# Kernel optimization log

Hardware: AMD Instinct MI355X
Metric: run time of the kernel (lower is better)

## Reference

```python
import jax, jax.numpy as jnp
import numpy as np

B, N, D, H = 4, 1024, 768, 12
DH = D // H
HIDDEN = 4 * D
EPS = 1e-6


def _layernorm(x, g, b):
    mu = jnp.mean(x, axis=-1, keepdims=True)
    var = jnp.mean(jnp.square(x - mu), axis=-1, keepdims=True)
    return (x - mu) * jax.lax.rsqrt(var + EPS) * g + b


def setup_inputs() -> dict:
    key = jax.random.key(0)
    ks = jax.random.split(key, 8)
    s = 0.02  # init scale for weights
    return {
        "x": jax.random.normal(ks[0], (B, N, D), jnp.float32),
        "adj_bias": jax.random.normal(ks[1], (N, N), jnp.float32) * 0.1,
        "ln1_g": jnp.ones((D,), jnp.float32),
        "ln1_b": jnp.zeros((D,), jnp.float32),
        "qkv_w": jax.random.normal(ks[2], (D, 3 * D), jnp.float32) * s,
        "qkv_b": jnp.zeros((3 * D,), jnp.float32),
        "proj_w": jax.random.normal(ks[3], (D, D), jnp.float32) * s,
        "proj_b": jnp.zeros((D,), jnp.float32),
        "ln2_g": jnp.ones((D,), jnp.float32),
        "ln2_b": jnp.zeros((D,), jnp.float32),
        "fc1_w": jax.random.normal(ks[4], (D, HIDDEN), jnp.float32) * s,
        "fc1_b": jnp.zeros((HIDDEN,), jnp.float32),
        "fc2_w": jax.random.normal(ks[5], (HIDDEN, D), jnp.float32) * s,
        "fc2_b": jnp.zeros((D,), jnp.float32),
    }


def reference(x, adj_bias, ln1_g, ln1_b, qkv_w, qkv_b, proj_w, proj_b,
              ln2_g, ln2_b, fc1_w, fc1_b, fc2_w, fc2_b):
    scale = DH ** -0.5
    # --- attention with additive adjacency bias ---
    h = _layernorm(x, ln1_g, ln1_b)
    qkv = (h @ qkv_w + qkv_b).reshape(B, N, 3, H, DH)
    q, k, v = (jnp.moveaxis(qkv, 2, 0)[i].transpose(0, 2, 1, 3) for i in range(3))  # [B,H,N,DH]
    scores = jnp.einsum('bhqd,bhkd->bhqk', q, k) * scale + adj_bias[None, None]
    w = jax.nn.softmax(scores, axis=-1)
    attn = jnp.einsum('bhqk,bhkd->bhqd', w, v)          # [B,H,N,DH]
    attn = attn.transpose(0, 2, 1, 3).reshape(B, N, D)  # [B,N,D]
    x = x + (attn @ proj_w + proj_b)
    # --- MLP ---
    h2 = _layernorm(x, ln2_g, ln2_b)
    m = jax.nn.gelu(h2 @ fc1_w + fc1_b, approximate=False) @ fc2_w + fc2_b
    return x + m
```

## Files before the change

kernel.cpp:

```cpp
#include <hip/hip_runtime.h>
#include <cstdint>
#include <cstring>

typedef unsigned short u16;
typedef __attribute__((ext_vector_type(8))) short short8;
typedef __attribute__((ext_vector_type(4))) float float4v;

#define BB 4
#define NN 1024
#define DD 768
#define HH 12
#define DHH 64
#define HID 3072
#define MM (BB*NN)

__device__ __forceinline__ u16 f2b(float f) {
  unsigned int u = __float_as_uint(f);
  u += 0x7FFF + ((u >> 16) & 1);
  return (u16)(u >> 16);
}
__device__ __forceinline__ float b2f(u16 h) {
  return __uint_as_float(((unsigned int)h) << 16);
}

__device__ __forceinline__ void gll16(const void* g, void* l) {
  __builtin_amdgcn_global_load_lds(
      (const __attribute__((address_space(1))) unsigned int*)g,
      (__attribute__((address_space(3))) unsigned int*)l, 16, 0, 0);
}

__global__ __launch_bounds__(256)
void prep_k(const float* __restrict__ qkvw, const float* __restrict__ projw,
            const float* __restrict__ fc1w, const float* __restrict__ fc2w,
            const float* __restrict__ adj,
            u16* __restrict__ wtqkv, u16* __restrict__ wtproj,
            u16* __restrict__ wtfc1, u16* __restrict__ wtfc2,
            u16* __restrict__ adjP) {
  __shared__ float tile[32][33];
  const int id = blockIdx.x, t = threadIdx.x;
  if (id < 6912) {
    const float* w; u16* wt; int K, N, tid;
    if (id < 1728)      { w = qkvw;  wt = wtqkv;  K = DD;  N = 3 * DD; tid = id; }
    else if (id < 2304) { w = projw; wt = wtproj; K = DD;  N = DD;     tid = id - 1728; }
    else if (id < 4608) { w = fc1w;  wt = wtfc1;  K = DD;  N = HID;    tid = id - 2304; }
    else                { w = fc2w;  wt = wtfc2;  K = HID; N = DD;     tid = id - 4608; }
    const int ntiles = N / 32;
    const int n0 = (tid % ntiles) * 32, k0 = (tid / ntiles) * 32;
    const int tx = t & 31, ty = t >> 5;
#pragma unroll
    for (int i = 0; i < 4; i++)
      tile[ty + i * 8][tx] = w[(size_t)(k0 + ty + i * 8) * N + n0 + tx];
    __syncthreads();
#pragma unroll
    for (int i = 0; i < 4; i++)
      wt[(size_t)(n0 + ty + i * 8) * K + k0 + tx] = f2b(tile[tx][ty + i * 8]);
  } else {
    const int aid = id - 6912;
    const int qt = aid >> 4, kt = aid & 15;
    const int wv = t >> 6, q4 = (t >> 4) & 3, m15 = t & 15;
    u16 v[16];
#pragma unroll
    for (int ct = 0; ct < 4; ct++)
#pragma unroll
      for (int r = 0; r < 4; r++)
        v[ct * 4 + r] =
            f2b(adj[(size_t)(qt * 64 + wv * 16 + q4 * 4 + r) * NN + kt * 64 + ct * 16 + m15]);
    u16* dst = adjP + (size_t)aid * 4096 + t * 16;
    *(uint4*)dst = *(const uint4*)&v[0];
    *(uint4*)(dst + 8) = *(const uint4*)&v[8];
  }
}

__global__ __launch_bounds__(256)
void ln_k(const float* __restrict__ x, const float* __restrict__ g,
          const float* __restrict__ b, u16* __restrict__ o) {
  const int row = blockIdx.x, t = threadIdx.x;
  const float* xr = x + (size_t)row * DD;
  float v0 = xr[t], v1 = xr[t + 256], v2 = xr[t + 512];
  float s = v0 + v1 + v2;
  float s2 = v0 * v0 + v1 * v1 + v2 * v2;
#pragma unroll
  for (int off = 32; off > 0; off >>= 1) {
    s += __shfl_down(s, off);
    s2 += __shfl_down(s2, off);
  }
  __shared__ float rs[4], rs2[4], bc[2];
  const int lane = t & 63, wv = t >> 6;
  if (lane == 0) { rs[wv] = s; rs2[wv] = s2; }
  __syncthreads();
  if (t == 0) {
    float ts = rs[0] + rs[1] + rs[2] + rs[3];
    float ts2 = rs2[0] + rs2[1] + rs2[2] + rs2[3];
    float mean = ts * (1.f / DD);
    float var = ts2 * (1.f / DD) - mean * mean;
    bc[0] = mean;
    bc[1] = rsqrtf(var + 1e-6f);
  }
  __syncthreads();
  const float mean = bc[0], rstd = bc[1];
  u16* orow = o + (size_t)row * DD;
  orow[t]       = f2b((v0 - mean) * rstd * g[t]       + b[t]);
  orow[t + 256] = f2b((v1 - mean) * rstd * g[t + 256] + b[t + 256]);
  orow[t + 512] = f2b((v2 - mean) * rstd * g[t + 512] + b[t + 512]);
}

template <int MODE, int TN>
__global__ __launch_bounds__(256, 4)
void gemm_k(const u16* __restrict__ A, const u16* __restrict__ Bt,
            const float* __restrict__ bias, const float* __restrict__ resid,
            float* __restrict__ outf, u16* __restrict__ outb,
            u16* __restrict__ outq, u16* __restrict__ outk, u16* __restrict__ outv,
            int M, int N, int K) {
  __shared__ u16 As[2][128 * 32];
  __shared__ u16 Bs[2][TN * 32];
  constexpr int JM = TN / 32;
  constexpr int VC = (TN == 128) ? 4 : 3;
  const int gx = gridDim.x;
  const int id = blockIdx.y * gx + blockIdx.x;
  const int xcd = id & 7, rem = id >> 3;
  const int bx = rem % gx, by = (rem / gx) * 8 + xcd;
  const int tileM = by * 128, tileN = bx * TN;
  const int lane = threadIdx.x & 63, wave = threadIdx.x >> 6;
  const int wrow = (wave >> 1) * 64, wcol = (wave & 1) * (TN / 2);
  const int m15 = lane & 15, q4 = lane >> 4;

  float4v acc[4][JM];
#pragma unroll
  for (int i = 0; i < 4; i++)
#pragma unroll
    for (int j = 0; j < JM; j++) acc[i][j] = (float4v)0.f;

  auto stage = [&](int kt, int buf) {
    const int kk0 = kt * 32;
#pragma unroll
    for (int q = wave; q < 8; q += 4) {
      const int c = q * 64 + lane;
      gll16(A + (size_t)(tileM + (c >> 2)) * K + kk0 + (c & 3) * 8, &As[buf][q * 512]);
    }
#pragma unroll
    for (int q = wave; q < TN / 16; q += 4) {
      const int c = q * 64 + lane;
      gll16(Bt + (size_t)(tileN + (c >> 2)) * K + kk0 + (c & 3) * 8, &Bs[buf][q * 512]);
    }
  };

  const int T = K >> 5;
  stage(0, 0);
  for (int kt = 0; kt < T; ++kt) {
    const int cur = kt & 1;
    if (kt + 1 < T) {
      stage(kt + 1, cur ^ 1);
      asm volatile("s_waitcnt vmcnt(%0)\n\ts_barrier" :: "n"(VC) : "memory");
    } else {
      asm volatile("s_waitcnt vmcnt(0)\n\ts_barrier" ::: "memory");
    }
    short8 af[4], bfr[JM];
#pragma unroll
    for (int i = 0; i < 4; i++)
      af[i] = *(const short8*)(&As[cur][(wrow + i * 16 + m15) * 32 + q4 * 8]);
#pragma unroll
    for (int j = 0; j < JM; j++)
      bfr[j] = *(const short8*)(&Bs[cur][(wcol + j * 16 + m15) * 32 + q4 * 8]);
#pragma unroll
    for (int i = 0; i < 4; i++)
#pragma unroll
      for (int j = 0; j < JM; j++)
        acc[i][j] = __builtin_amdgcn_mfma_f32_16x16x32_bf16(af[i], bfr[j], acc[i][j], 0, 0, 0);
    asm volatile("s_waitcnt lgkmcnt(0)\n\ts_barrier" ::: "memory");
  }

#pragma unroll
  for (int i = 0; i < 4; i++) {
#pragma unroll
    for (int j = 0; j < JM; j++) {
      const int col = tileN + wcol + j * 16 + m15;
#pragma unroll
      for (int r = 0; r < 4; r++) {
        const int row = tileM + wrow + i * 16 + q4 * 4 + r;
        float v = acc[i][j][r] + bias[col];
        if (MODE == 1) {
          outf[(size_t)row * N + col] = resid[(size_t)row * N + col] + v;
        } else if (MODE == 2) {
          float gv = 0.5f * v * (1.f + erff(v * 0.70710678f));
          outb[(size_t)row * N + col] = f2b(gv);
        } else {
          const int three = col / DD, hh = (col % DD) >> 6, dh = col & 63;
          const int bb = row >> 10, nn = row & 1023;
          if (three == 2) {
            outv[(((size_t)(bb * HH + hh)) * DHH + dh) * NN + nn] = f2b(v);
          } else {
            const size_t idx = (((size_t)(bb * HH + hh)) * NN + nn) * DHH + dh;
            (three == 0 ? outq : outk)[idx] = f2b(v);
          }
        }
      }
    }
  }
}

__global__ __launch_bounds__(256, 4)
void attn_k(const u16* __restrict__ qw, const u16* __restrict__ kw,
            const u16* __restrict__ vtw, const u16* __restrict__ adjP,
            u16* __restrict__ out) {
  __shared__ u16 Ks[64][72];
  __shared__ u16 Vt[64][72];
  __shared__ u16 Pb[4][16][72];

  const int id = blockIdx.y * 16 + blockIdx.x;
  const int xcd = id & 7, rem = id >> 3;
  const int qt = rem % 16, bh = (rem / 16) * 8 + xcd;
  const int t = threadIdx.x, lane = t & 63, wave = t >> 6;
  const int m15 = lane & 15, q4 = lane >> 4;

  const u16* qrow = qw + ((size_t)bh * NN + qt * 64 + wave * 16 + m15) * DHH;
  const short8 qf0 = *(const short8*)(qrow + q4 * 8);
  const short8 qf1 = *(const short8*)(qrow + 32 + q4 * 8);

  float lreg[4] = {0.f, 0.f, 0.f, 0.f};
  float4v o[4];
#pragma unroll
  for (int ct = 0; ct < 4; ct++) o[ct] = (float4v)0.f;

  const u16* kbase0 = kw + (size_t)bh * NN * DHH;
  const u16* vtbase0 = vtw + (size_t)bh * DHH * NN;
  const u16* abase = adjP + (size_t)qt * 16 * 4096 + t * 16;

  const int r0 = t >> 3;
  const int c80 = (t & 7) * 8;

  uint4 kr0 = *(const uint4*)(kbase0 + r0 * 64 + c80);
  uint4 kr1 = *(const uint4*)(kbase0 + (r0 + 32) * 64 + c80);
  uint4 vr0 = *(const uint4*)(vtbase0 + (size_t)r0 * NN + c80);
  uint4 vr1 = *(const uint4*)(vtbase0 + (size_t)(r0 + 32) * NN + c80);

  for (int kt = 0; kt < 16; kt++) {
    __syncthreads();
    *(uint4*)&Ks[r0][c80] = kr0;
    *(uint4*)&Ks[r0 + 32][c80] = kr1;
    *(uint4*)&Vt[r0][c80] = vr0;
    *(uint4*)&Vt[r0 + 32][c80] = vr1;
    __syncthreads();
    if (kt < 15) {
      const u16* kb = kbase0 + (size_t)(kt + 1) * 64 * DHH;
      const u16* vb = vtbase0 + (kt + 1) * 64;
      kr0 = *(const uint4*)(kb + r0 * 64 + c80);
      kr1 = *(const uint4*)(kb + (r0 + 32) * 64 + c80);
      vr0 = *(const uint4*)(vb + (size_t)r0 * NN + c80);
      vr1 = *(const uint4*)(vb + (size_t)(r0 + 32) * NN + c80);
    }
    u16 av[16];
    const u16* ap = abase + (size_t)kt * 4096;
    *(uint4*)&av[0] = *(const uint4*)ap;
    *(uint4*)&av[8] = *(const uint4*)(ap + 8);

    float4v s[4];
#pragma unroll
    for (int ct = 0; ct < 4; ct++) s[ct] = (float4v)0.f;
#pragma unroll
    for (int ct = 0; ct < 4; ct++) {
      short8 b = *(const short8*)&Ks[ct * 16 + m15][q4 * 8];
      s[ct] = __builtin_amdgcn_mfma_f32_16x16x32_bf16(qf0, b, s[ct], 0, 0, 0);
    }
#pragma unroll
    for (int ct = 0; ct < 4; ct++) {
      short8 b = *(const short8*)&Ks[ct * 16 + m15][32 + q4 * 8];
      s[ct] = __builtin_amdgcn_mfma_f32_16x16x32_bf16(qf1, b, s[ct], 0, 0, 0);
    }

#pragma unroll
    for (int ct = 0; ct < 4; ct++)
#pragma unroll
      for (int r = 0; r < 4; r++) {
        float v = s[ct][r] * 0.125f + b2f(av[ct * 4 + r]);
        u16 pb = f2b(__expf(v));
        Pb[wave][q4 * 4 + r][ct * 16 + m15] = pb;
        lreg[r] += b2f(pb);
      }

    asm volatile("s_waitcnt lgkmcnt(0)" ::: "memory");

    short8 a0 = *(const short8*)&Pb[wave][m15][q4 * 8];
    short8 a1 = *(const short8*)&Pb[wave][m15][32 + q4 * 8];
#pragma unroll
    for (int ct = 0; ct < 4; ct++) {
      short8 b = *(const short8*)&Vt[ct * 16 + m15][q4 * 8];
      o[ct] = __builtin_amdgcn_mfma_f32_16x16x32_bf16(a0, b, o[ct], 0, 0, 0);
    }
#pragma unroll
    for (int ct = 0; ct < 4; ct++) {
      short8 b = *(const short8*)&Vt[ct * 16 + m15][32 + q4 * 8];
      o[ct] = __builtin_amdgcn_mfma_f32_16x16x32_bf16(a1, b, o[ct], 0, 0, 0);
    }
  }

#pragma unroll
  for (int off = 1; off < 16; off <<= 1)
#pragma unroll
    for (int r = 0; r < 4; r++) lreg[r] += __shfl_xor(lreg[r], off);

  const int bb2 = bh / HH, hh = bh % HH;
  const int row0 = qt * 64 + wave * 16 + q4 * 4;
#pragma unroll
  for (int ct = 0; ct < 4; ct++)
#pragma unroll
    for (int r = 0; r < 4; r++)
      out[((size_t)(bb2 * NN + row0 + r)) * DD + hh * 64 + ct * 16 + m15] =
          f2b(o[ct][r] / lreg[r]);
}

extern "C" void kernel_launch(void* const* d_in, const int* in_sizes, int n_in,
                              void* d_out, int out_size, void* d_ws, size_t ws_size,
                              hipStream_t stream) {
  const float* x     = (const float*)d_in[0];
  const float* adj   = (const float*)d_in[1];
  const float* ln1g  = (const float*)d_in[2];
  const float* ln1b  = (const float*)d_in[3];
  const float* qkvw  = (const float*)d_in[4];
  const float* qkvb  = (const float*)d_in[5];
  const float* projw = (const float*)d_in[6];
  const float* projb = (const float*)d_in[7];
  const float* ln2g  = (const float*)d_in[8];
  const float* ln2b  = (const float*)d_in[9];
  const float* fc1w  = (const float*)d_in[10];
  const float* fc1b  = (const float*)d_in[11];
  const float* fc2w  = (const float*)d_in[12];
  const float* fc2b  = (const float*)d_in[13];
  float* out = (float*)d_out;

  char* ws = (char*)d_ws;
  u16* wtqkv = (u16*)ws;  ws += (size_t)DD * (3 * DD) * 2;
  u16* wtproj = (u16*)ws; ws += (size_t)DD * DD * 2;
  u16* wtfc1 = (u16*)ws;  ws += (size_t)DD * HID * 2;
  u16* wtfc2 = (u16*)ws;  ws += (size_t)HID * DD * 2;
  u16* adjP = (u16*)ws;   ws += (size_t)NN * NN * 2;
  u16* hbuf = (u16*)ws;   ws += (size_t)MM * DD * 2;
  u16* qws = (u16*)ws;    ws += (size_t)MM * DD * 2;
  u16* kws = (u16*)ws;    ws += (size_t)MM * DD * 2;
  u16* vtws = (u16*)ws;   ws += (size_t)MM * DD * 2;
  u16* attnb = (u16*)ws;  ws += (size_t)MM * DD * 2;
  u16* h2buf = (u16*)ws;  ws += (size_t)MM * DD * 2;
  u16* a1buf = (u16*)ws;  ws += (size_t)MM * HID * 2;

  prep_k<<<7168, 256, 0, stream>>>(qkvw, projw, fc1w, fc2w, adj,
                                   wtqkv, wtproj, wtfc1, wtfc2, adjP);

  ln_k<<<MM, 256, 0, stream>>>(x, ln1g, ln1b, hbuf);

  gemm_k<0, 128><<<dim3((3 * DD) / 128, MM / 128), 256, 0, stream>>>(
      hbuf, wtqkv, qkvb, nullptr, nullptr, nullptr, qws, kws, vtws, MM, 3 * DD, DD);

  attn_k<<<dim3(NN / 64, BB * HH), 256, 0, stream>>>(qws, kws, vtws, adjP, attnb);

  gemm_k<1, 64><<<dim3(DD / 64, MM / 128), 256, 0, stream>>>(
      attnb, wtproj, projb, x, out, nullptr, nullptr, nullptr, nullptr, MM, DD, DD);

  ln_k<<<MM, 256, 0, stream>>>(out, ln2g, ln2b, h2buf);

  gemm_k<2, 128><<<dim3(HID / 128, MM / 128), 256, 0, stream>>>(
      h2buf, wtfc1, fc1b, nullptr, nullptr, a1buf, nullptr, nullptr, nullptr, MM, HID, DD);

  gemm_k<1, 64><<<dim3(DD / 64, MM / 128), 256, 0, stream>>>(
      a1buf, wtfc2, fc2b, out, out, nullptr, nullptr, nullptr, nullptr, MM, DD, HID);
}
```

Measured before the change: 294.2 us.

## Split-K narrow GEMMs with atomic accumulation and register-staged tile loads

The proj and fc2 GEMMs now use split-K (2 and 4 chunks) and accumulate into the output with float atomics. A separate init kernel first writes residual plus bias into the output buffer. The aim is more blocks on the narrow N=768 GEMMs, which previously launched only 384 blocks. The GEMM mainloop also switches from direct global-to-LDS loads to a two-deep register prefetch followed by LDS stores, and occupancy bounds change for the TN=128 variant. The cost is extra atomic traffic, two added elementwise passes, nondeterministic summation order, and a different load pipeline that may hide latency less well.

```diff
diff --git a/kernel.cpp b/kernel.cpp
--- a/kernel.cpp
+++ b/kernel.cpp
@@ -21,12 +21,6 @@
 }
 __device__ __forceinline__ float b2f(u16 h) {
   return __uint_as_float(((unsigned int)h) << 16);
-}
-
-__device__ __forceinline__ void gll16(const void* g, void* l) {
-  __builtin_amdgcn_global_load_lds(
-      (const __attribute__((address_space(1))) unsigned int*)g,
-      (__attribute__((address_space(3))) unsigned int*)l, 16, 0, 0);
 }
 
 __global__ __launch_bounds__(256)
@@ -104,69 +98,86 @@
   orow[t + 512] = f2b((v2 - mean) * rstd * g[t + 512] + b[t + 512]);
 }
 
+__global__ __launch_bounds__(256)
+void init_out_k(const float* resid, const float* __restrict__ bias, float* out) {
+  const int total = MM * DD / 4;
+  const float4* r4 = (const float4*)resid;
+  const float4* b4 = (const float4*)bias;
+  float4* o4 = (float4*)out;
+  for (int i = blockIdx.x * 256 + threadIdx.x; i < total; i += gridDim.x * 256) {
+    float4 a = r4[i], b = b4[i % (DD / 4)];
+    o4[i] = make_float4(a.x + b.x, a.y + b.y, a.z + b.z, a.w + b.w);
+  }
+}
+
 template <int MODE, int TN>
-__global__ __launch_bounds__(256, 4)
+__global__ __launch_bounds__(256, (TN == 64) ? 4 : 3)
 void gemm_k(const u16* __restrict__ A, const u16* __restrict__ Bt,
-            const float* __restrict__ bias, const float* __restrict__ resid,
+            const float* __restrict__ bias,
             float* __restrict__ outf, u16* __restrict__ outb,
             u16* __restrict__ outq, u16* __restrict__ outk, u16* __restrict__ outv,
             int M, int N, int K) {
+  constexpr int JM = TN / 32;
+  constexpr int LB = TN / 64;
   __shared__ u16 As[2][128 * 32];
   __shared__ u16 Bs[2][TN * 32];
-  constexpr int JM = TN / 32;
-  constexpr int VC = (TN == 128) ? 4 : 3;
   const int gx = gridDim.x;
   const int id = blockIdx.y * gx + blockIdx.x;
   const int xcd = id & 7, rem = id >> 3;
   const int bx = rem % gx, by = (rem / gx) * 8 + xcd;
   const int tileM = by * 128, tileN = bx * TN;
+  const int Kc = K / (int)gridDim.z;
+  const int k0 = blockIdx.z * Kc;
+  const int T = Kc >> 5;
   const int lane = threadIdx.x & 63, wave = threadIdx.x >> 6;
   const int wrow = (wave >> 1) * 64, wcol = (wave & 1) * (TN / 2);
   const int m15 = lane & 15, q4 = lane >> 4;
 
+  const int c0 = wave * 64 + lane, c1 = (wave + 4) * 64 + lane;
+  const u16* Aa0 = A + (size_t)(tileM + (c0 >> 2)) * K + k0 + (c0 & 3) * 8;
+  const u16* Aa1 = A + (size_t)(tileM + (c1 >> 2)) * K + k0 + (c1 & 3) * 8;
+  const u16* Ba0 = Bt + (size_t)(tileN + (c0 >> 2)) * K + k0 + (c0 & 3) * 8;
+  const u16* Ba1 = Bt + (size_t)(tileN + ((LB == 2 ? c1 : c0) >> 2)) * K + k0 +
+                   ((LB == 2 ? c1 : c0) & 3) * 8;
+
   float4v acc[4][JM];
 #pragma unroll
   for (int i = 0; i < 4; i++)
 #pragma unroll
     for (int j = 0; j < JM; j++) acc[i][j] = (float4v)0.f;
 
-  auto stage = [&](int kt, int buf) {
-    const int kk0 = kt * 32;
-#pragma unroll
-    for (int q = wave; q < 8; q += 4) {
-      const int c = q * 64 + lane;
-      gll16(A + (size_t)(tileM + (c >> 2)) * K + kk0 + (c & 3) * 8, &As[buf][q * 512]);
-    }
-#pragma unroll
-    for (int q = wave; q < TN / 16; q += 4) {
-      const int c = q * 64 + lane;
-      gll16(Bt + (size_t)(tileN + (c >> 2)) * K + kk0 + (c & 3) * 8, &Bs[buf][q * 512]);
-    }
+  uint4 ra[2][2], rb[2][LB];
+  auto load = [&](int kt) {
+    const int s = kt & 1;
+    const size_t o = (size_t)kt * 32;
+    ra[s][0] = *(const uint4*)(Aa0 + o);
+    ra[s][1] = *(const uint4*)(Aa1 + o);
+    rb[s][0] = *(const uint4*)(Ba0 + o);
+    if (LB == 2) rb[s][1] = *(const uint4*)(Ba1 + o);
   };
 
-  const int T = K >> 5;
-  stage(0, 0);
+  load(0);
+  if (T > 1) load(1);
   for (int kt = 0; kt < T; ++kt) {
-    const int cur = kt & 1;
-    if (kt + 1 < T) {
-      stage(kt + 1, cur ^ 1);
-      asm volatile("s_waitcnt vmcnt(%0)\n\ts_barrier" :: "n"(VC) : "memory");
-    } else {
-      asm volatile("s_waitcnt vmcnt(0)\n\ts_barrier" ::: "memory");
-    }
+    const int buf = kt & 1, s = kt & 1;
+    *(uint4*)&As[buf][wave * 512 + lane * 8] = ra[s][0];
+    *(uint4*)&As[buf][(wave + 4) * 512 + lane * 8] = ra[s][1];
+    *(uint4*)&Bs[buf][wave * 512 + lane * 8] = rb[s][0];
+    if (LB == 2) *(uint4*)&Bs[buf][(wave + 4) * 512 + lane * 8] = rb[s][1];
+    if (kt + 2 < T) load(kt + 2);
+    asm volatile("s_waitcnt lgkmcnt(0)\n\ts_barrier" ::: "memory");
     short8 af[4], bfr[JM];
 #pragma unroll
     for (int i = 0; i < 4; i++)
-      af[i] = *(const short8*)(&As[cur][(wrow + i * 16 + m15) * 32 + q4 * 8]);
+      af[i] = *(const short8*)(&As[buf][(wrow + i * 16 + m15) * 32 + q4 * 8]);
 #pragma unroll
     for (int j = 0; j < JM; j++)
-      bfr[j] = *(const short8*)(&Bs[cur][(wcol + j * 16 + m15) * 32 + q4 * 8]);
+      bfr[j] = *(const short8*)(&Bs[buf][(wcol + j * 16 + m15) * 32 + q4 * 8]);
 #pragma unroll
     for (int i = 0; i < 4; i++)
 #pragma unroll
       for (int j = 0; j < JM; j++)
         acc[i][j] = __builtin_amdgcn_mfma_f32_16x16x32_bf16(af[i], bfr[j], acc[i][j], 0, 0, 0);
-    asm volatile("s_waitcnt lgkmcnt(0)\n\ts_barrier" ::: "memory");
   }
 
 #pragma unroll
@@ -177,13 +188,15 @@
 #pragma unroll
       for (int r = 0; r < 4; r++) {
         const int row = tileM + wrow + i * 16 + q4 * 4 + r;
-        float v = acc[i][j][r] + bias[col];
+        float v = acc[i][j][r];
         if (MODE == 1) {
-          outf[(size_t)row * N + col] = resid[(size_t)row * N + col] + v;
+          atomicAdd(&outf[(size_t)row * N + col], v);
         } else if (MODE == 2) {
+          v += bias[col];
           float gv = 0.5f * v * (1.f + erff(v * 0.70710678f));
           outb[(size_t)row * N + col] = f2b(gv);
         } else {
+          v += bias[col];
           const int three = col / DD, hh = (col % DD) >> 6, dh = col & 63;
           const int bb = row >> 10, nn = row & 1023;
           if (three == 2) {
@@ -346,19 +359,21 @@
 
   ln_k<<<MM, 256, 0, stream>>>(x, ln1g, ln1b, hbuf);
 
-  gemm_k<0, 128><<<dim3((3 * DD) / 128, MM / 128), 256, 0, stream>>>(
-      hbuf, wtqkv, qkvb, nullptr, nullptr, nullptr, qws, kws, vtws, MM, 3 * DD, DD);
-
-  attn_k<<<dim3(NN / 64, BB * HH), 256, 0, stream>>>(qws, kws, vtws, adjP, attnb);
-
-  gemm_k<1, 64><<<dim3(DD / 64, MM / 128), 256, 0, stream>>>(
-      attnb, wtproj, projb, x, out, nullptr, nullptr, nullptr, nullptr, MM, DD, DD);
+  gemm_k<0, 128><<<dim3(18, 32, 1), 256, 0, stream>>>(
+      hbuf, wtqkv, qkvb, nullptr, nullptr, qws, kws, vtws, MM, 3 * DD, DD);
+
+  attn_k<<<dim3(16, 48), 256, 0, stream>>>(qws, kws, vtws, adjP, attnb);
+
+  init_out_k<<<768, 256, 0, stream>>>(x, projb, out);
+  gemm_k<1, 64><<<dim3(12, 32, 2), 256, 0, stream>>>(
+      attnb, wtproj, nullptr, out, nullptr, nullptr, nullptr, nullptr, MM, DD, DD);
 
   ln_k<<<MM, 256, 0, stream>>>(out, ln2g, ln2b, h2buf);
 
-  gemm_k<2, 128><<<dim3(HID / 128, MM / 128), 256, 0, stream>>>(
-      h2buf, wtfc1, fc1b, nullptr, nullptr, a1buf, nullptr, nullptr, nullptr, MM, HID, DD);
-
-  gemm_k<1, 64><<<dim3(DD / 64, MM / 128), 256, 0, stream>>>(
-      a1buf, wtfc2, fc2b, out, out, nullptr, nullptr, nullptr, nullptr, MM, DD, HID);
-}
+  gemm_k<2, 128><<<dim3(24, 32, 1), 256, 0, stream>>>(
+      h2buf, wtfc1, fc1b, nullptr, a1buf, nullptr, nullptr, nullptr, MM, HID, DD);
+
+  init_out_k<<<768, 256, 0, stream>>>(out, fc2b, out);
+  gemm_k<1, 64><<<dim3(12, 32, 4), 256, 0, stream>>>(
+      a1buf, wtfc2, nullptr, out, nullptr, nullptr, nullptr, nullptr, MM, DD, HID);
+}
```

Result: slower. 554.2 us (+88.4%).

## Stage GEMM tiles through registers with two-deep prefetch and smaller tiles for N=768

Applied to the files above, without the earlier changes.

Replaces the direct global-to-LDS async loads in the GEMM with register-staged loads that prefetch two K-steps ahead, then write to LDS each iteration, using a single barrier per step. It also templates the M tile size so the proj and fc2 GEMMs use 64x64 tiles (more blocks, higher occupancy bound), while the QKV and fc1 GEMMs keep 128x128 with a lower occupancy hint. The aim is to hide global latency better and fill the GPU for the narrow-N GEMMs. The cost is extra VGPRs for staging, and the LDS write/read sharing a buffer with only one barrier could race across iterations.

```diff
diff --git a/kernel.cpp b/kernel.cpp
--- a/kernel.cpp
+++ b/kernel.cpp
@@ -21,12 +21,6 @@
 }
 __device__ __forceinline__ float b2f(u16 h) {
   return __uint_as_float(((unsigned int)h) << 16);
-}
-
-__device__ __forceinline__ void gll16(const void* g, void* l) {
-  __builtin_amdgcn_global_load_lds(
-      (const __attribute__((address_space(1))) unsigned int*)g,
-      (__attribute__((address_space(3))) unsigned int*)l, 16, 0, 0);
 }
 
 __global__ __launch_bounds__(256)
@@ -104,73 +98,83 @@
   orow[t + 512] = f2b((v2 - mean) * rstd * g[t + 512] + b[t + 512]);
 }
 
-template <int MODE, int TN>
-__global__ __launch_bounds__(256, 4)
+template <int MODE, int TM, int TN>
+__global__ __launch_bounds__(256, (TM == 64) ? 6 : 3)
 void gemm_k(const u16* __restrict__ A, const u16* __restrict__ Bt,
             const float* __restrict__ bias, const float* __restrict__ resid,
             float* __restrict__ outf, u16* __restrict__ outb,
             u16* __restrict__ outq, u16* __restrict__ outk, u16* __restrict__ outv,
             int M, int N, int K) {
-  __shared__ u16 As[2][128 * 32];
+  constexpr int IM = TM / 32;
+  constexpr int JM = TN / 32;
+  constexpr int LA = TM / 64;
+  constexpr int LB = TN / 64;
+  __shared__ u16 As[2][TM * 32];
   __shared__ u16 Bs[2][TN * 32];
-  constexpr int JM = TN / 32;
-  constexpr int VC = (TN == 128) ? 4 : 3;
   const int gx = gridDim.x;
   const int id = blockIdx.y * gx + blockIdx.x;
   const int xcd = id & 7, rem = id >> 3;
   const int bx = rem % gx, by = (rem / gx) * 8 + xcd;
-  const int tileM = by * 128, tileN = bx * TN;
+  const int tileM = by * TM, tileN = bx * TN;
+  const int T = K >> 5;
   const int lane = threadIdx.x & 63, wave = threadIdx.x >> 6;
-  const int wrow = (wave >> 1) * 64, wcol = (wave & 1) * (TN / 2);
+  const int wrow = (wave >> 1) * (TM / 2), wcol = (wave & 1) * (TN / 2);
   const int m15 = lane & 15, q4 = lane >> 4;
 
-  float4v acc[4][JM];
-#pragma unroll
-  for (int i = 0; i < 4; i++)
+  const int c0 = wave * 64 + lane;
+  const u16* Aa[LA];
+  const u16* Ba[LB];
+#pragma unroll
+  for (int p = 0; p < LA; p++)
+    Aa[p] = A + (size_t)(tileM + (c0 >> 2) + 64 * p) * K + (c0 & 3) * 8;
+#pragma unroll
+  for (int p = 0; p < LB; p++)
+    Ba[p] = Bt + (size_t)(tileN + (c0 >> 2) + 64 * p) * K + (c0 & 3) * 8;
+
+  float4v acc[IM][JM];
+#pragma unroll
+  for (int i = 0; i < IM; i++)
 #pragma unroll
     for (int j = 0; j < JM; j++) acc[i][j] = (float4v)0.f;
 
-  auto stage = [&](int kt, int buf) {
-    const int kk0 = kt * 32;
-#pragma unroll
-    for (int q = wave; q < 8; q += 4) {
-      const int c = q * 64 + lane;
-      gll16(A + (size_t)(tileM + (c >> 2)) * K + kk0 + (c & 3) * 8, &As[buf][q * 512]);
-    }
-#pragma unroll
-    for (int q = wave; q < TN / 16; q += 4) {
-      const int c = q * 64 + lane;
-      gll16(Bt + (size_t)(tileN + (c >> 2)) * K + kk0 + (c & 3) * 8, &Bs[buf][q * 512]);
-    }
+  uint4 ra[2][LA], rb[2][LB];
+  auto load = [&](int kt) {
+    const int s = kt & 1;
+    const size_t o = (size_t)kt * 32;
+#pragma unroll
+    for (int p = 0; p < LA; p++) ra[s][p] = *(const uint4*)(Aa[p] + o);
+#pragma unroll
+    for (int p = 0; p < LB; p++) rb[s][p] = *(const uint4*)(Ba[p] + o);
   };
 
-  const int T = K >> 5;
-  stage(0, 0);
+  load(0);
+  if (T > 1) load(1);
   for (int kt = 0; kt < T; ++kt) {
-    const int cur = kt & 1;
-    if (kt + 1 < T) {
-      stage(kt + 1, cur ^ 1);
-      asm volatile("s_waitcnt vmcnt(%0)\n\ts_barrier" :: "n"(VC) : "memory");
-    } else {
-      asm volatile("s_waitcnt vmcnt(0)\n\ts_barrier" ::: "memory");
-    }
-    short8 af[4], bfr[JM];
-#pragma unroll
-    for (int i = 0; i < 4; i++)
-      af[i] = *(const short8*)(&As[cur][(wrow + i * 16 + m15) * 32 + q4 * 8]);
+    const int buf = kt & 1, s = kt & 1;
+#pragma unroll
+    for (int p = 0; p < LA; p++)
+      *(uint4*)&As[buf][(wave + 4 * p) * 512 + lane * 8] = ra[s][p];
+#pragma unroll
+    for (int p = 0; p < LB; p++)
+      *(uint4*)&Bs[buf][(wave + 4 * p) * 512 + lane * 8] = rb[s][p];
+    if (kt + 2 < T) load(kt + 2);
+    asm volatile("s_waitcnt lgkmcnt(0)\n\ts_barrier" ::: "memory");
+    short8 af[IM], bfr[JM];
+#pragma unroll
+    for (int i = 0; i < IM; i++)
+      af[i] = *(const short8*)(&As[buf][(wrow + i * 16 + m15) * 32 + q4 * 8]);
 #pragma unroll
     for (int j = 0; j < JM; j++)
-      bfr[j] = *(const short8*)(&Bs[cur][(wcol + j * 16 + m15) * 32 + q4 * 8]);
-#pragma unroll
-    for (int i = 0; i < 4; i++)
+      bfr[j] = *(const short8*)(&Bs[buf][(wcol + j * 16 + m15) * 32 + q4 * 8]);
+#pragma unroll
+    for (int i = 0; i < IM; i++)
 #pragma unroll
       for (int j = 0; j < JM; j++)
         acc[i][j] = __builtin_amdgcn_mfma_f32_16x16x32_bf16(af[i], bfr[j], acc[i][j], 0, 0, 0);
-    asm volatile("s_waitcnt lgkmcnt(0)\n\ts_barrier" ::: "memory");
-  }
-
-#pragma unroll
-  for (int i = 0; i < 4; i++) {
+  }
+
+#pragma unroll
+  for (int i = 0; i < IM; i++) {
 #pragma unroll
     for (int j = 0; j < JM; j++) {
       const int col = tileN + wcol + j * 16 + m15;
@@ -346,19 +350,19 @@
 
   ln_k<<<MM, 256, 0, stream>>>(x, ln1g, ln1b, hbuf);
 
-  gemm_k<0, 128><<<dim3((3 * DD) / 128, MM / 128), 256, 0, stream>>>(
+  gemm_k<0, 128, 128><<<dim3(18, 32), 256, 0, stream>>>(
       hbuf, wtqkv, qkvb, nullptr, nullptr, nullptr, qws, kws, vtws, MM, 3 * DD, DD);
 
-  attn_k<<<dim3(NN / 64, BB * HH), 256, 0, stream>>>(qws, kws, vtws, adjP, attnb);
-
-  gemm_k<1, 64><<<dim3(DD / 64, MM / 128), 256, 0, stream>>>(
+  attn_k<<<dim3(16, 48), 256, 0, stream>>>(qws, kws, vtws, adjP, attnb);
+
+  gemm_k<1, 64, 64><<<dim3(12, 64), 256, 0, stream>>>(
       attnb, wtproj, projb, x, out, nullptr, nullptr, nullptr, nullptr, MM, DD, DD);
 
   ln_k<<<MM, 256, 0, stream>>>(out, ln2g, ln2b, h2buf);
 
-  gemm_k<2, 128><<<dim3(HID / 128, MM / 128), 256, 0, stream>>>(
+  gemm_k<2, 128, 128><<<dim3(24, 32), 256, 0, stream>>>(
       h2buf, wtfc1, fc1b, nullptr, nullptr, a1buf, nullptr, nullptr, nullptr, MM, HID, DD);
 
-  gemm_k<1, 64><<<dim3(DD / 64, MM / 128), 256, 0, stream>>>(
+  gemm_k<1, 64, 64><<<dim3(12, 64), 256, 0, stream>>>(
       a1buf, wtfc2, fc2b, out, out, nullptr, nullptr, nullptr, nullptr, MM, DD, HID);
 }
```

Measured after the change: 562.1 us. 91.1% more time.
